# Performance work log

Measured on AMD Instinct MI355X. Metric: run time of the kernel, lower is better.

Reference implementation:

```python
import jax, jax.numpy as jnp
import numpy as np

B = 4096        # number of motif graphs in the batch
H = 256         # hidden_channels
P = 128         # num_prototypes
V = 2000        # motif vocab size (embedding table has V+1 rows)
N_ATOMS = 32768 # focal context atoms
N_RES = 262144  # residues
KNN = 4         # construct_num_neighbors (and cos_sim topk)
DIST_TH = 6.0


def setup_inputs() -> dict:
    key = jax.random.key(0)
    ks = jax.random.split(key, 14)
    return {
        "h_ctx_focal": jax.random.normal(ks[0], (N_ATOMS, H), jnp.float32),
        "pos_ctx_focal": jax.random.normal(ks[1], (N_ATOMS, 3), jnp.float32) * 5.0,
        "h_residue": jax.random.normal(ks[2], (N_RES, H), jnp.float32),
        "residue_pos": jax.random.normal(ks[3], (N_RES, 3, 3), jnp.float32) * 3.0,
        "embedding_weight": jax.random.normal(ks[4], (V + 1, H), jnp.float32) * 0.02,
        "prototypes": jax.random.normal(ks[5], (P, H), jnp.float32),
        "prototype_count": jax.random.uniform(ks[6], (P, V), jnp.float32) * 10.0,
        "motif_w": jax.random.normal(ks[7], (3 * H, H), jnp.float32) * 0.02,
        "motif_b": jnp.zeros((H,), jnp.float32),
        "gnn_w1": jax.random.normal(ks[8], (H, H), jnp.float32) * 0.05,
        "gnn_w2": jax.random.normal(ks[9], (H, H), jnp.float32) * 0.05,
        "current_wid": jax.random.randint(ks[10], (B,), 0, V),
        "current_atoms_batch": jnp.sort(jax.random.randint(ks[11], (N_ATOMS,), 0, B)),
        "amino_acid_batch": jnp.sort(jax.random.randint(ks[12], (N_RES,), 0, B)),
    }


def _l2norm(x, axis=-1):
    # F.normalize: x / max(||x||, eps)
    n = jnp.linalg.norm(x, axis=axis, keepdims=True)
    return x / jnp.maximum(n, 1e-12)


def reference(h_ctx_focal, pos_ctx_focal, h_residue, residue_pos,
              embedding_weight, prototypes, prototype_count,
              motif_w, motif_b, gnn_w1, gnn_w2,
              current_wid, current_atoms_batch, amino_acid_batch):
    # --- scatter-based motif aggregation (forward_motif) ---
    node_hiddens = jax.ops.segment_sum(h_ctx_focal, current_atoms_batch, num_segments=B)
    motif_hiddens = embedding_weight[current_wid]                       # [B,H]
    pos_sum = jax.ops.segment_sum(pos_ctx_focal, current_atoms_batch, num_segments=B)
    cnt = jax.ops.segment_sum(jnp.ones((N_ATOMS,), pos_ctx_focal.dtype),
                              current_atoms_batch, num_segments=B)
    center_pos = pos_sum / jnp.maximum(cnt, 1.0)[:, None]               # scatter_mean [B,3]

    # distance-thresholded residue gather-reduce (CA atom = index 1)
    ca = residue_pos[:, 1, :]                                           # [N_RES,3]
    dist = jnp.linalg.norm(ca - center_pos[amino_acid_batch], axis=1)
    rmask = (dist < DIST_TH).astype(h_residue.dtype)                    # [N_RES]
    residue_emb = jax.ops.segment_sum(h_residue * rmask[:, None],
                                      amino_acid_batch, num_segments=B)  # [B,H]

    # --- MGraph.output: prototype kNN graph + prototype->motif tf-idf edges ---
    cos = _l2norm(residue_emb) @ _l2norm(prototypes).T                  # [B,P]
    _, knn_idx = jax.lax.top_k(cos, KNN)                                # [B,KNN]
    dim = B + P + V
    adj = jnp.zeros((dim, dim), residue_emb.dtype)
    ind1 = knn_idx.T.reshape(-1) + B
    ind0 = jnp.tile(jnp.arange(B), KNN)
    adj = adj.at[ind0, ind1].set(1.0)
    sum_proto = jnp.sum(prototype_count, axis=1, keepdims=True)         # [P,1]
    sum_motif = jnp.sum((prototype_count > 0).astype(jnp.float32), axis=0)  # [V]
    block = prototype_count / (sum_proto + 1.0) * (
        jnp.log((1.0 + P) / (1.0 + sum_motif)) + 1.0)                   # [P,V]
    adj = adj.at[B:B + P, B + P:].set(block)
    A = adj + adj.T  # edge duplication with swapped indices == symmetrize

    # --- WeightGNN (2-layer weighted message passing over the motif graph) ---
    node_feat = jnp.concatenate([residue_emb, prototypes, embedding_weight[:V]], axis=0)
    h1 = jax.nn.relu((A @ node_feat) @ gnn_w1)
    residue_out = ((A @ h1) @ gnn_w2)[:B]                               # [B,H]

    # --- prediction head ---
    pred_vecs = jnp.concatenate([0.8 * node_hiddens,
                                 0.7 * motif_hiddens,
                                 1.5 * residue_out], axis=-1)           # [B,3H]
    pred_scores = (pred_vecs @ motif_w + motif_b) @ embedding_weight.T  # [B,V+1]
    return pred_scores
```

## Files before the change

### kernel.cpp

```cpp
#include <hip/hip_runtime.h>
#include <hip/hip_bf16.h>
#include <math.h>

#define NB 4096
#define HD 256
#define NP 128
#define NV 2000
#define NATOMS 32768
#define NRES 262144
#define VCHUNK 125

typedef __attribute__((ext_vector_type(8))) short bf16x8;
typedef __attribute__((ext_vector_type(4))) float f32x4;
typedef __attribute__((ext_vector_type(8))) unsigned short u16x8;

__device__ __forceinline__ unsigned short f2bf(float f) {
  unsigned int u = __builtin_bit_cast(unsigned int, f);
  u += 0x7FFFu + ((u >> 16) & 1u);
  return (unsigned short)(u >> 16);
}
__device__ __forceinline__ float bf2f(unsigned short h) {
  unsigned int u = ((unsigned int)h) << 16;
  return __builtin_bit_cast(float, u);
}

#define I_SP   128
#define I_WL   (I_SP + 8)
#define I_PR   (I_WL + 128)
#define I_HZ   (I_PR + 128)
#define I_ES   (I_HZ + 512)
#define I_MS   (I_ES + 192)
#define I_AS   (I_MS + 128)
#define I_RS   (I_AS + 1024)

__global__ __launch_bounds__(256) void k_init0(
    const int* __restrict__ ab, const int* __restrict__ rb,
    const float* __restrict__ pcnt, const float* __restrict__ proto,
    const float* __restrict__ emb, const float* __restrict__ mw,
    float* __restrict__ inv_sp, float* __restrict__ wl, float* __restrict__ pnT,
    float* __restrict__ hin,
    unsigned short* __restrict__ embH, unsigned short* __restrict__ embL,
    unsigned short* __restrict__ mwTH, unsigned short* __restrict__ mwTL,
    int* __restrict__ astart, int* __restrict__ rstart) {
  int blk = blockIdx.x, t = threadIdx.x;
  __shared__ float red[256];
  if (blk < I_SP) {
    int p = blk;
    float s = 0.f;
    for (int v = t; v < NV; v += 256) s += pcnt[(size_t)p * NV + v];
    red[t] = s; __syncthreads();
    for (int off = 128; off; off >>= 1) { if (t < off) red[t] += red[t + off]; __syncthreads(); }
    if (!t) inv_sp[p] = 1.0f / (red[0] + 1.0f);
  } else if (blk < I_WL) {
    int v = (blk - I_SP) * 256 + t;
    if (v < NV) {
      float sm = 0.f;
      for (int p = 0; p < NP; ++p) sm += (pcnt[(size_t)p * NV + v] > 0.f) ? 1.f : 0.f;
      wl[v] = logf((1.0f + NP) / (1.0f + sm)) + 1.0f;
    }
  } else if (blk < I_PR) {
    int p = blk - I_WL;
    float x = proto[p * HD + t];
    red[t] = x * x; __syncthreads();
    for (int off = 128; off; off >>= 1) { if (t < off) red[t] += red[t + off]; __syncthreads(); }
    float inv = 1.0f / fmaxf(sqrtf(red[0]), 1e-12f);
    pnT[t * NP + p] = x * inv;
  } else if (blk < I_HZ) {
    hin[(blk - I_PR) * 256 + t] = 0.f;
  } else if (blk < I_ES) {
    int e0 = ((blk - I_HZ) * 256 + t) * 4;
#pragma unroll
    for (int j = 0; j < 4; ++j) {
      int e = e0 + j;
      if (e < 2001 * HD) {
        float x = emb[e];
        unsigned short h = f2bf(x);
        embH[e] = h; embL[e] = f2bf(x - bf2f(h));
      } else {
        embH[e] = 0; embL[e] = 0;
      }
    }
  } else if (blk < I_MS) {
    int e0 = ((blk - I_ES) * 256 + t) * 4;
#pragma unroll
    for (int j = 0; j < 4; ++j) {
      int e = e0 + j;
      int n = e / 768, k = e - n * 768;
      float x = mw[(size_t)k * HD + n];
      unsigned short h = f2bf(x);
      mwTH[e] = h; mwTL[e] = f2bf(x - bf2f(h));
    }
  } else if (blk < I_AS) {
    int i = (blk - I_MS) * 256 + t;
    int cur = ab[i];
    int prev = (i == 0) ? -1 : ab[i - 1];
    for (int b = prev + 1; b <= cur; ++b) astart[b] = i;
    if (i == NATOMS - 1)
      for (int b = cur + 1; b <= NB; ++b) astart[b] = NATOMS;
  } else {
    int i = (blk - I_AS) * 256 + t;
    int cur = rb[i];
    int prev = (i == 0) ? -1 : rb[i - 1];
    for (int b = prev + 1; b <= cur; ++b) rstart[b] = i;
    if (i == NRES - 1)
      for (int b = cur + 1; b <= NB; ++b) rstart[b] = NRES;
  }
}

__global__ __launch_bounds__(256) void k_mega(
    const float* __restrict__ hctx, const float* __restrict__ pos,
    const float* __restrict__ hres, const float* __restrict__ rpos,
    const int* __restrict__ astart, const int* __restrict__ rstart,
    const float* __restrict__ pcnt, const float* __restrict__ wl,
    const float* __restrict__ inv_sp, const float* __restrict__ emb,
    const float* __restrict__ pnT,
    float* __restrict__ nh, int* __restrict__ knn, float* __restrict__ hin) {
  int blk = blockIdx.x, t = threadIdx.x;
  __shared__ int lst[256];
  __shared__ int cnt;
  __shared__ float cw[VCHUNK];
  __shared__ float sre[HD];
  __shared__ float part[256];
  __shared__ float c[NP];
  __shared__ float rv[256];
  __shared__ int ri[256];
  __shared__ int kk[4];
  __shared__ float scen[3];
  if (blk < NB) {
    int b = blk;
    int s = astart[b], e = astart[b + 1];
    {
      float a0 = 0.f, a1 = 0.f, a2 = 0.f, a3 = 0.f;
      int a = s;
      for (; a + 3 < e; a += 4) {
        a0 += hctx[(size_t)(a + 0) * HD + t];
        a1 += hctx[(size_t)(a + 1) * HD + t];
        a2 += hctx[(size_t)(a + 2) * HD + t];
        a3 += hctx[(size_t)(a + 3) * HD + t];
      }
      for (; a < e; ++a) a0 += hctx[(size_t)a * HD + t];
      nh[(size_t)b * HD + t] = (a0 + a1) + (a2 + a3);
      if (t < 3) {
        float ps = 0.f;
        for (int aa = s; aa < e; ++aa) ps += pos[aa * 3 + t];
        scen[t] = ps / fmaxf((float)(e - s), 1.0f);
      }
    }
    __syncthreads();
    float c0 = scen[0], c1 = scen[1], c2 = scen[2];
    int rs = rstart[b], re_ = rstart[b + 1];
    float a0 = 0.f, a1 = 0.f, a2 = 0.f, a3 = 0.f, a4 = 0.f, a5 = 0.f, a6 = 0.f, a7 = 0.f;
    for (int cc = rs; cc < re_; cc += 256) {
      if (!t) cnt = 0;
      __syncthreads();
      int r = cc + t;
      if (r < re_) {
        float dx = rpos[(size_t)r * 9 + 3] - c0;
        float dy = rpos[(size_t)r * 9 + 4] - c1;
        float dz = rpos[(size_t)r * 9 + 5] - c2;
        if (dx * dx + dy * dy + dz * dz < 36.0f) {
          int j = atomicAdd(&cnt, 1);
          lst[j] = r;
        }
      }
      __syncthreads();
      int n = cnt;
      int j = 0;
      for (; j + 7 < n; j += 8) {
        a0 += hres[(size_t)lst[j + 0] * HD + t];
        a1 += hres[(size_t)lst[j + 1] * HD + t];
        a2 += hres[(size_t)lst[j + 2] * HD + t];
        a3 += hres[(size_t)lst[j + 3] * HD + t];
        a4 += hres[(size_t)lst[j + 4] * HD + t];
        a5 += hres[(size_t)lst[j + 5] * HD + t];
        a6 += hres[(size_t)lst[j + 6] * HD + t];
        a7 += hres[(size_t)lst[j + 7] * HD + t];
      }
      for (; j < n; ++j) a0 += hres[(size_t)lst[j] * HD + t];
      __syncthreads();
    }
    float acc = ((a0 + a1) + (a2 + a3)) + ((a4 + a5) + (a6 + a7));
    sre[t] = acc;
    part[t] = acc * acc;
    __syncthreads();
    for (int off = 128; off; off >>= 1) { if (t < off) part[t] += part[t + off]; __syncthreads(); }
    float invn = 1.0f / fmaxf(sqrtf(part[0]), 1e-12f);
    __syncthreads();
    int p = t & 127, half = t >> 7;
    float d = 0.f;
    int h0 = half * 128;
#pragma unroll 8
    for (int h = h0; h < h0 + 128; ++h) d += sre[h] * pnT[h * NP + p];
    part[t] = d;
    __syncthreads();
    if (t < NP) c[t] = (part[t] + part[t + 128]) * invn;
    __syncthreads();
    for (int k = 0; k < 4; ++k) {
      rv[t] = (t < NP) ? c[t] : -INFINITY;
      ri[t] = t;
      __syncthreads();
      for (int off = 128; off; off >>= 1) {
        if (t < off) {
          float ov = rv[t + off]; int oi = ri[t + off];
          if (ov > rv[t] || (ov == rv[t] && oi < ri[t])) { rv[t] = ov; ri[t] = oi; }
        }
        __syncthreads();
      }
      if (!t) { knn[b * 4 + k] = ri[0]; kk[k] = ri[0]; }
      if (t == ri[0]) c[t] = -INFINITY;
      __syncthreads();
    }
#pragma unroll
    for (int k = 0; k < 4; ++k) atomicAdd(&hin[kk[k] * HD + t], sre[t]);
  } else {
    int pc = blk - NB;
    int p = pc >> 4, ch = pc & 15;
    int v0 = ch * VCHUNK;
    float isp = inv_sp[p];
    for (int v = t; v < VCHUNK; v += 256) cw[v] = pcnt[(size_t)p * NV + v0 + v] * wl[v0 + v] * isp;
    __syncthreads();
    float acc = 0.f;
#pragma unroll 8
    for (int v = 0; v < VCHUNK; ++v) acc += cw[v] * emb[(size_t)(v0 + v) * HD + t];
    atomicAdd(&hin[p * HD + t], acc);
  }
}

__global__ __launch_bounds__(256) void k_h1hw(const float* __restrict__ hin,
                                              const float* __restrict__ w1,
                                              const float* __restrict__ w2,
                                              float* __restrict__ hw) {
  int p = blockIdx.x, t = threadIdx.x;
  __shared__ float s[HD], s2[HD];
  s[t] = hin[p * HD + t];
  __syncthreads();
  float a = 0.f;
#pragma unroll 8
  for (int h = 0; h < HD; ++h) a += s[h] * w1[h * HD + t];
  s2[t] = fmaxf(a, 0.f);
  __syncthreads();
  float o = 0.f;
#pragma unroll 8
  for (int h = 0; h < HD; ++h) o += s2[h] * w2[h * HD + t];
  hw[p * HD + t] = o;
}

__global__ __launch_bounds__(512) void k_gemm1(
    const float* __restrict__ nh, const float* __restrict__ emb,
    const int* __restrict__ wid, const int* __restrict__ knn, const float* __restrict__ hw,
    const unsigned short* __restrict__ mwTH, const unsigned short* __restrict__ mwTL,
    const float* __restrict__ mb,
    unsigned short* __restrict__ tbH, unsigned short* __restrict__ tbL) {
  __shared__ __align__(16) unsigned short Ah[64][40], Al[64][40], Bh[64][40], Bl[64][40];
  __shared__ int swid[64];
  __shared__ int4 sknn[64];
  int tid = threadIdx.x, lane = tid & 63, w = tid >> 6;
  int wm = (w & 1) * 32, wn = (w >> 1) * 16;
  int bm = blockIdx.x * 64, bn = blockIdx.y * 64;
  if (tid < 64) { swid[tid] = wid[bm + tid]; sknn[tid] = ((const int4*)knn)[bm + tid]; }
  f32x4 acc[2] = {};
  for (int k0 = 0; k0 < 768; k0 += 32) {
    __syncthreads();
    for (int i = tid; i < 2048; i += 512) {
      int m = i >> 5, k = i & 31;
      float x;
      if (k0 < 256) {
        x = 0.8f * nh[(size_t)(bm + m) * HD + k0 + k];
      } else if (k0 < 512) {
        x = 0.7f * emb[(size_t)swid[m] * HD + (k0 - 256) + k];
      } else {
        int4 kn = sknn[m];
        int kk2 = (k0 - 512) + k;
        x = 1.5f * (hw[kn.x * HD + kk2] + hw[kn.y * HD + kk2] +
                    hw[kn.z * HD + kk2] + hw[kn.w * HD + kk2]);
      }
      unsigned short h = f2bf(x);
      Ah[m][k] = h; Al[m][k] = f2bf(x - bf2f(h));
    }
    if (tid < 256) {
      int e = tid * 8, n = e >> 5, k = e & 31;
      size_t idx = (size_t)(bn + n) * 768 + k0 + k;
      *(u16x8*)&Bh[n][k] = *(const u16x8*)&mwTH[idx];
      *(u16x8*)&Bl[n][k] = *(const u16x8*)&mwTL[idx];
    }
    __syncthreads();
    int r = lane & 15, kb = (lane >> 4) * 8;
    bf16x8 bh = *(const bf16x8*)&Bh[wn + r][kb];
    bf16x8 bl = *(const bf16x8*)&Bl[wn + r][kb];
#pragma unroll
    for (int i = 0; i < 2; ++i) {
      bf16x8 ah = *(const bf16x8*)&Ah[wm + i * 16 + r][kb];
      bf16x8 al = *(const bf16x8*)&Al[wm + i * 16 + r][kb];
      acc[i] = __builtin_amdgcn_mfma_f32_16x16x32_bf16(ah, bh, acc[i], 0, 0, 0);
      acc[i] = __builtin_amdgcn_mfma_f32_16x16x32_bf16(ah, bl, acc[i], 0, 0, 0);
      acc[i] = __builtin_amdgcn_mfma_f32_16x16x32_bf16(al, bh, acc[i], 0, 0, 0);
    }
  }
  int col0 = lane & 15, row0 = (lane >> 4) * 4;
  int col = bn + wn + col0;
  float bv = mb[col];
#pragma unroll
  for (int i = 0; i < 2; ++i)
#pragma unroll
    for (int rr = 0; rr < 4; ++rr) {
      int row = bm + wm + i * 16 + row0 + rr;
      float x = acc[i][rr] + bv;
      unsigned short h = f2bf(x);
      tbH[(size_t)row * HD + col] = h;
      tbL[(size_t)row * HD + col] = f2bf(x - bf2f(h));
    }
}

__global__ __launch_bounds__(256) void k_gemm2(
    const unsigned short* __restrict__ tbH, const unsigned short* __restrict__ tbL,
    const unsigned short* __restrict__ embH, const unsigned short* __restrict__ embL,
    float* __restrict__ out) {
  __shared__ __align__(16) unsigned short AH[128][40], AL[128][40], BH[128][40], BL[128][40];
  int tid = threadIdx.x, lane = tid & 63, w = tid >> 6;
  int wm = (w & 1) * 64, wn = (w >> 1) * 64;
  int orig = blockIdx.x;
  int swz = (orig & 7) * 64 + (orig >> 3);
  int bm = (swz & 31) * 128, bn = (swz >> 5) * 128;
  f32x4 acc[4][4] = {};
  for (int k0 = 0; k0 < HD; k0 += 32) {
    __syncthreads();
#pragma unroll
    for (int cch = 0; cch < 2; ++cch) {
      int e = (tid + cch * 256) * 8;
      int m = e >> 5, k = e & 31;
      *(u16x8*)&AH[m][k] = *(const u16x8*)&tbH[(size_t)(bm + m) * HD + k0 + k];
      *(u16x8*)&AL[m][k] = *(const u16x8*)&tbL[(size_t)(bm + m) * HD + k0 + k];
      *(u16x8*)&BH[m][k] = *(const u16x8*)&embH[(size_t)(bn + m) * HD + k0 + k];
      *(u16x8*)&BL[m][k] = *(const u16x8*)&embL[(size_t)(bn + m) * HD + k0 + k];
    }
    __syncthreads();
    int r = lane & 15, kb = (lane >> 4) * 8;
    bf16x8 ah[4], al[4], bh[4], bl[4];
#pragma unroll
    for (int i = 0; i < 4; ++i) {
      ah[i] = *(const bf16x8*)&AH[wm + i * 16 + r][kb];
      al[i] = *(const bf16x8*)&AL[wm + i * 16 + r][kb];
      bh[i] = *(const bf16x8*)&BH[wn + i * 16 + r][kb];
      bl[i] = *(const bf16x8*)&BL[wn + i * 16 + r][kb];
    }
#pragma unroll
    for (int i = 0; i < 4; ++i)
#pragma unroll
      for (int j = 0; j < 4; ++j) {
        acc[i][j] = __builtin_amdgcn_mfma_f32_16x16x32_bf16(ah[i], bh[j], acc[i][j], 0, 0, 0);
        acc[i][j] = __builtin_amdgcn_mfma_f32_16x16x32_bf16(ah[i], bl[j], acc[i][j], 0, 0, 0);
        acc[i][j] = __builtin_amdgcn_mfma_f32_16x16x32_bf16(al[i], bh[j], acc[i][j], 0, 0, 0);
      }
  }
  int col0 = lane & 15, row0 = (lane >> 4) * 4;
#pragma unroll
  for (int i = 0; i < 4; ++i)
#pragma unroll
    for (int j = 0; j < 4; ++j) {
      int col = bn + wn + j * 16 + col0;
      if (col <= 2000) {
#pragma unroll
        for (int rr = 0; rr < 4; ++rr) {
          int row = bm + wm + i * 16 + row0 + rr;
          out[(size_t)row * 2001 + col] = acc[i][j][rr];
        }
      }
    }
}

extern "C" void kernel_launch(void* const* d_in, const int* in_sizes, int n_in,
                              void* d_out, int out_size, void* d_ws, size_t ws_size,
                              hipStream_t stream) {
  const float* hctx  = (const float*)d_in[0];
  const float* pos   = (const float*)d_in[1];
  const float* hres  = (const float*)d_in[2];
  const float* rpos  = (const float*)d_in[3];
  const float* emb   = (const float*)d_in[4];
  const float* proto = (const float*)d_in[5];
  const float* pcnt  = (const float*)d_in[6];
  const float* mw    = (const float*)d_in[7];
  const float* mb    = (const float*)d_in[8];
  const float* w1    = (const float*)d_in[9];
  const float* w2    = (const float*)d_in[10];
  const int* wid     = (const int*)d_in[11];
  const int* ab      = (const int*)d_in[12];
  const int* rb      = (const int*)d_in[13];
  float* out = (float*)d_out;

  float* ws     = (float*)d_ws;
  float* nh     = ws;
  float* inv_sp = nh + (size_t)NB * HD;
  float* wl     = inv_sp + 128;
  float* pnT    = wl + 2048;
  float* hin    = pnT + NP * HD;
  float* hw     = hin + NP * HD;
  int*   knn    = (int*)(hw + NP * HD);
  int*   astart = knn + NB * 4;
  int*   rstart = astart + 4104;
  unsigned short* tbH  = (unsigned short*)(rstart + 4104);
  unsigned short* tbL  = tbH + (size_t)NB * HD;
  unsigned short* embH = tbL + (size_t)NB * HD;
  unsigned short* embL = embH + (size_t)2048 * HD;
  unsigned short* mwTH = embL + (size_t)2048 * HD;
  unsigned short* mwTL = mwTH + (size_t)768 * HD;

  k_init0<<<I_RS, 256, 0, stream>>>(ab, rb, pcnt, proto, emb, mw,
                                    inv_sp, wl, pnT, hin,
                                    embH, embL, mwTH, mwTL, astart, rstart);
  k_mega<<<NB + NP * 16, 256, 0, stream>>>(hctx, pos, hres, rpos, astart, rstart,
                                           pcnt, wl, inv_sp, emb, pnT, nh, knn, hin);
  k_h1hw<<<NP, 256, 0, stream>>>(hin, w1, w2, hw);
  k_gemm1<<<dim3(NB / 64, 4), 512, 0, stream>>>(nh, emb, wid, knn, hw,
                                                mwTH, mwTL, mb, tbH, tbL);
  k_gemm2<<<512, 256, 0, stream>>>(tbH, tbL, embH, embL, out);
}
```

Measured before the change: 534.9 us.

## Use wave shuffles in top-k, split gemm1 prologue, double-buffer both GEMMs

New measurement: 513.9 us. 3.9% less time.

```diff
diff --git a/kernel.cpp b/kernel.cpp
--- a/kernel.cpp
+++ b/kernel.cpp
@@ -122,12 +122,12 @@
   __shared__ float sre[HD];
   __shared__ float part[256];
   __shared__ float c[NP];
-  __shared__ float rv[256];
-  __shared__ int ri[256];
+  __shared__ float wsum[4];
   __shared__ int kk[4];
   __shared__ float scen[3];
   if (blk < NB) {
     int b = blk;
+    int lane = t & 63, w = t >> 6;
     int s = astart[b], e = astart[b + 1];
     {
       float a0 = 0.f, a1 = 0.f, a2 = 0.f, a3 = 0.f;
@@ -181,11 +181,12 @@
     }
     float acc = ((a0 + a1) + (a2 + a3)) + ((a4 + a5) + (a6 + a7));
     sre[t] = acc;
-    part[t] = acc * acc;
-    __syncthreads();
-    for (int off = 128; off; off >>= 1) { if (t < off) part[t] += part[t + off]; __syncthreads(); }
-    float invn = 1.0f / fmaxf(sqrtf(part[0]), 1e-12f);
-    __syncthreads();
+    float ss = acc * acc;
+#pragma unroll
+    for (int off = 32; off; off >>= 1) ss += __shfl_xor(ss, off);
+    if (!lane) wsum[w] = ss;
+    __syncthreads();
+    float invn = 1.0f / fmaxf(sqrtf((wsum[0] + wsum[1]) + (wsum[2] + wsum[3])), 1e-12f);
     int p = t & 127, half = t >> 7;
     float d = 0.f;
     int h0 = half * 128;
@@ -195,21 +196,24 @@
     __syncthreads();
     if (t < NP) c[t] = (part[t] + part[t + 128]) * invn;
     __syncthreads();
-    for (int k = 0; k < 4; ++k) {
-      rv[t] = (t < NP) ? c[t] : -INFINITY;
-      ri[t] = t;
-      __syncthreads();
-      for (int off = 128; off; off >>= 1) {
-        if (t < off) {
-          float ov = rv[t + off]; int oi = ri[t + off];
-          if (ov > rv[t] || (ov == rv[t] && oi < ri[t])) { rv[t] = ov; ri[t] = oi; }
+    if (t < 64) {
+      float v0 = c[t], v1 = c[t + 64];
+#pragma unroll
+      for (int k = 0; k < 4; ++k) {
+        float bv = v0; int bi = t;
+        if (v1 > bv) { bv = v1; bi = t + 64; }
+#pragma unroll
+        for (int off = 32; off; off >>= 1) {
+          float ov = __shfl_xor(bv, off);
+          int oi = __shfl_xor(bi, off);
+          if (ov > bv || (ov == bv && oi < bi)) { bv = ov; bi = oi; }
         }
-        __syncthreads();
-      }
-      if (!t) { knn[b * 4 + k] = ri[0]; kk[k] = ri[0]; }
-      if (t == ri[0]) c[t] = -INFINITY;
-      __syncthreads();
-    }
+        if (!t) { knn[b * 4 + k] = bi; kk[k] = bi; }
+        if (bi == t) v0 = -INFINITY;
+        if (bi == t + 64) v1 = -INFINITY;
+      }
+    }
+    __syncthreads();
 #pragma unroll
     for (int k = 0; k < 4; ++k) atomicAdd(&hin[kk[k] * HD + t], sre[t]);
   } else {
@@ -245,69 +249,83 @@
   hw[p * HD + t] = o;
 }
 
-__global__ __launch_bounds__(512) void k_gemm1(
+__global__ __launch_bounds__(256) void k_prepU(
     const float* __restrict__ nh, const float* __restrict__ emb,
     const int* __restrict__ wid, const int* __restrict__ knn, const float* __restrict__ hw,
+    unsigned short* __restrict__ uH, unsigned short* __restrict__ uL) {
+  int b = blockIdx.x, t = threadIdx.x;
+  size_t base = (size_t)b * 768;
+  float x0 = 0.8f * nh[(size_t)b * HD + t];
+  float x1 = 0.7f * emb[(size_t)wid[b] * HD + t];
+  int4 kn = ((const int4*)knn)[b];
+  float x2 = 1.5f * (hw[kn.x * HD + t] + hw[kn.y * HD + t] +
+                     hw[kn.z * HD + t] + hw[kn.w * HD + t]);
+  unsigned short h;
+  h = f2bf(x0); uH[base + t] = h;       uL[base + t] = f2bf(x0 - bf2f(h));
+  h = f2bf(x1); uH[base + 256 + t] = h; uL[base + 256 + t] = f2bf(x1 - bf2f(h));
+  h = f2bf(x2); uH[base + 512 + t] = h; uL[base + 512 + t] = f2bf(x2 - bf2f(h));
+}
+
+__global__ __launch_bounds__(256) void k_gemm1(
+    const unsigned short* __restrict__ uH, const unsigned short* __restrict__ uL,
     const unsigned short* __restrict__ mwTH, const unsigned short* __restrict__ mwTL,
     const float* __restrict__ mb,
     unsigned short* __restrict__ tbH, unsigned short* __restrict__ tbL) {
-  __shared__ __align__(16) unsigned short Ah[64][40], Al[64][40], Bh[64][40], Bl[64][40];
-  __shared__ int swid[64];
-  __shared__ int4 sknn[64];
+  __shared__ __align__(16) unsigned short AH[2][64][40], AL[2][64][40],
+                                          BH[2][64][40], BL[2][64][40];
   int tid = threadIdx.x, lane = tid & 63, w = tid >> 6;
-  int wm = (w & 1) * 32, wn = (w >> 1) * 16;
+  int wm = (w & 1) * 32, wn = (w >> 1) * 32;
   int bm = blockIdx.x * 64, bn = blockIdx.y * 64;
-  if (tid < 64) { swid[tid] = wid[bm + tid]; sknn[tid] = ((const int4*)knn)[bm + tid]; }
-  f32x4 acc[2] = {};
-  for (int k0 = 0; k0 < 768; k0 += 32) {
-    __syncthreads();
-    for (int i = tid; i < 2048; i += 512) {
-      int m = i >> 5, k = i & 31;
-      float x;
-      if (k0 < 256) {
-        x = 0.8f * nh[(size_t)(bm + m) * HD + k0 + k];
-      } else if (k0 < 512) {
-        x = 0.7f * emb[(size_t)swid[m] * HD + (k0 - 256) + k];
-      } else {
-        int4 kn = sknn[m];
-        int kk2 = (k0 - 512) + k;
-        x = 1.5f * (hw[kn.x * HD + kk2] + hw[kn.y * HD + kk2] +
-                    hw[kn.z * HD + kk2] + hw[kn.w * HD + kk2]);
-      }
-      unsigned short h = f2bf(x);
-      Ah[m][k] = h; Al[m][k] = f2bf(x - bf2f(h));
-    }
-    if (tid < 256) {
-      int e = tid * 8, n = e >> 5, k = e & 31;
-      size_t idx = (size_t)(bn + n) * 768 + k0 + k;
-      *(u16x8*)&Bh[n][k] = *(const u16x8*)&mwTH[idx];
-      *(u16x8*)&Bl[n][k] = *(const u16x8*)&mwTL[idx];
-    }
-    __syncthreads();
+  f32x4 acc[2][2] = {};
+#define G1_STAGE(bf, kt)                                                        \
+  {                                                                             \
+    int e = tid * 8, m = e >> 5, k = e & 31;                                    \
+    size_t ia = (size_t)(bm + m) * 768 + (kt) * 32 + k;                         \
+    size_t ib = (size_t)(bn + m) * 768 + (kt) * 32 + k;                         \
+    *(u16x8*)&AH[bf][m][k] = *(const u16x8*)&uH[ia];                            \
+    *(u16x8*)&AL[bf][m][k] = *(const u16x8*)&uL[ia];                            \
+    *(u16x8*)&BH[bf][m][k] = *(const u16x8*)&mwTH[ib];                          \
+    *(u16x8*)&BL[bf][m][k] = *(const u16x8*)&mwTL[ib];                          \
+  }
+  G1_STAGE(0, 0);
+  __syncthreads();
+  for (int kt = 0; kt < 24; ++kt) {
+    int cur = kt & 1;
+    if (kt + 1 < 24) G1_STAGE(cur ^ 1, kt + 1);
     int r = lane & 15, kb = (lane >> 4) * 8;
-    bf16x8 bh = *(const bf16x8*)&Bh[wn + r][kb];
-    bf16x8 bl = *(const bf16x8*)&Bl[wn + r][kb];
+    bf16x8 ah[2], al[2], bh[2], bl[2];
 #pragma unroll
     for (int i = 0; i < 2; ++i) {
-      bf16x8 ah = *(const bf16x8*)&Ah[wm + i * 16 + r][kb];
-      bf16x8 al = *(const bf16x8*)&Al[wm + i * 16 + r][kb];
-      acc[i] = __builtin_amdgcn_mfma_f32_16x16x32_bf16(ah, bh, acc[i], 0, 0, 0);
-      acc[i] = __builtin_amdgcn_mfma_f32_16x16x32_bf16(ah, bl, acc[i], 0, 0, 0);
-      acc[i] = __builtin_amdgcn_mfma_f32_16x16x32_bf16(al, bh, acc[i], 0, 0, 0);
-    }
+      ah[i] = *(const bf16x8*)&AH[cur][wm + i * 16 + r][kb];
+      al[i] = *(const bf16x8*)&AL[cur][wm + i * 16 + r][kb];
+      bh[i] = *(const bf16x8*)&BH[cur][wn + i * 16 + r][kb];
+      bl[i] = *(const bf16x8*)&BL[cur][wn + i * 16 + r][kb];
+    }
+#pragma unroll
+    for (int i = 0; i < 2; ++i)
+#pragma unroll
+      for (int j = 0; j < 2; ++j) {
+        acc[i][j] = __builtin_amdgcn_mfma_f32_16x16x32_bf16(ah[i], bh[j], acc[i][j], 0, 0, 0);
+        acc[i][j] = __builtin_amdgcn_mfma_f32_16x16x32_bf16(ah[i], bl[j], acc[i][j], 0, 0, 0);
+        acc[i][j] = __builtin_amdgcn_mfma_f32_16x16x32_bf16(al[i], bh[j], acc[i][j], 0, 0, 0);
+      }
+    __syncthreads();
   }
   int col0 = lane & 15, row0 = (lane >> 4) * 4;
-  int col = bn + wn + col0;
-  float bv = mb[col];
 #pragma unroll
   for (int i = 0; i < 2; ++i)
 #pragma unroll
-    for (int rr = 0; rr < 4; ++rr) {
-      int row = bm + wm + i * 16 + row0 + rr;
-      float x = acc[i][rr] + bv;
-      unsigned short h = f2bf(x);
-      tbH[(size_t)row * HD + col] = h;
-      tbL[(size_t)row * HD + col] = f2bf(x - bf2f(h));
+    for (int j = 0; j < 2; ++j) {
+      int col = bn + wn + j * 16 + col0;
+      float bv = mb[col];
+#pragma unroll
+      for (int rr = 0; rr < 4; ++rr) {
+        int row = bm + wm + i * 16 + row0 + rr;
+        float x = acc[i][j][rr] + bv;
+        unsigned short h = f2bf(x);
+        tbH[(size_t)row * HD + col] = h;
+        tbL[(size_t)row * HD + col] = f2bf(x - bf2f(h));
+      }
     }
 }
 
@@ -315,33 +333,41 @@
     const unsigned short* __restrict__ tbH, const unsigned short* __restrict__ tbL,
     const unsigned short* __restrict__ embH, const unsigned short* __restrict__ embL,
     float* __restrict__ out) {
-  __shared__ __align__(16) unsigned short AH[128][40], AL[128][40], BH[128][40], BL[128][40];
+  __shared__ __align__(16) unsigned short AH[2][128][40], AL[2][128][40],
+                                          BH[2][128][40], BL[2][128][40];
   int tid = threadIdx.x, lane = tid & 63, w = tid >> 6;
   int wm = (w & 1) * 64, wn = (w >> 1) * 64;
   int orig = blockIdx.x;
   int swz = (orig & 7) * 64 + (orig >> 3);
   int bm = (swz & 31) * 128, bn = (swz >> 5) * 128;
   f32x4 acc[4][4] = {};
-  for (int k0 = 0; k0 < HD; k0 += 32) {
-    __syncthreads();
-#pragma unroll
-    for (int cch = 0; cch < 2; ++cch) {
-      int e = (tid + cch * 256) * 8;
-      int m = e >> 5, k = e & 31;
-      *(u16x8*)&AH[m][k] = *(const u16x8*)&tbH[(size_t)(bm + m) * HD + k0 + k];
-      *(u16x8*)&AL[m][k] = *(const u16x8*)&tbL[(size_t)(bm + m) * HD + k0 + k];
-      *(u16x8*)&BH[m][k] = *(const u16x8*)&embH[(size_t)(bn + m) * HD + k0 + k];
-      *(u16x8*)&BL[m][k] = *(const u16x8*)&embL[(size_t)(bn + m) * HD + k0 + k];
-    }
-    __syncthreads();
+#define G2_STAGE(bf, kt)                                                        \
+  {                                                                             \
+    _Pragma("unroll")                                                           \
+    for (int cch = 0; cch < 2; ++cch) {                                         \
+      int e = (tid + cch * 256) * 8;                                            \
+      int m = e >> 5, k = e & 31;                                               \
+      size_t ia = (size_t)(bm + m) * HD + (kt) * 32 + k;                        \
+      size_t ib = (size_t)(bn + m) * HD + (kt) * 32 + k;                        \
+      *(u16x8*)&AH[bf][m][k] = *(const u16x8*)&tbH[ia];                         \
+      *(u16x8*)&AL[bf][m][k] = *(const u16x8*)&tbL[ia];                         \
+      *(u16x8*)&BH[bf][m][k] = *(const u16x8*)&embH[ib];                        \
+      *(u16x8*)&BL[bf][m][k] = *(const u16x8*)&embL[ib];                        \
+    }                                                                           \
+  }
+  G2_STAGE(0, 0);
+  __syncthreads();
+  for (int kt = 0; kt < 8; ++kt) {
+    int cur = kt & 1;
+    if (kt + 1 < 8) G2_STAGE(cur ^ 1, kt + 1);
     int r = lane & 15, kb = (lane >> 4) * 8;
     bf16x8 ah[4], al[4], bh[4], bl[4];
 #pragma unroll
     for (int i = 0; i < 4; ++i) {
-      ah[i] = *(const bf16x8*)&AH[wm + i * 16 + r][kb];
-      al[i] = *(const bf16x8*)&AL[wm + i * 16 + r][kb];
-      bh[i] = *(const bf16x8*)&BH[wn + i * 16 + r][kb];
-      bl[i] = *(const bf16x8*)&BL[wn + i * 16 + r][kb];
+      ah[i] = *(const bf16x8*)&AH[cur][wm + i * 16 + r][kb];
+      al[i] = *(const bf16x8*)&AL[cur][wm + i * 16 + r][kb];
+      bh[i] = *(const bf16x8*)&BH[cur][wn + i * 16 + r][kb];
+      bl[i] = *(const bf16x8*)&BL[cur][wn + i * 16 + r][kb];
     }
 #pragma unroll
     for (int i = 0; i < 4; ++i)
@@ -351,6 +377,7 @@
         acc[i][j] = __builtin_amdgcn_mfma_f32_16x16x32_bf16(ah[i], bl[j], acc[i][j], 0, 0, 0);
         acc[i][j] = __builtin_amdgcn_mfma_f32_16x16x32_bf16(al[i], bh[j], acc[i][j], 0, 0, 0);
       }
+    __syncthreads();
   }
   int col0 = lane & 15, row0 = (lane >> 4) * 4;
 #pragma unroll
@@ -403,6 +430,8 @@
   unsigned short* embL = embH + (size_t)2048 * HD;
   unsigned short* mwTH = embL + (size_t)2048 * HD;
   unsigned short* mwTL = mwTH + (size_t)768 * HD;
+  unsigned short* uH   = mwTL + (size_t)768 * HD;
+  unsigned short* uL   = uH + (size_t)NB * 768;
 
   k_init0<<<I_RS, 256, 0, stream>>>(ab, rb, pcnt, proto, emb, mw,
                                     inv_sp, wl, pnT, hin,
@@ -410,7 +439,7 @@
   k_mega<<<NB + NP * 16, 256, 0, stream>>>(hctx, pos, hres, rpos, astart, rstart,
                                            pcnt, wl, inv_sp, emb, pnT, nh, knn, hin);
   k_h1hw<<<NP, 256, 0, stream>>>(hin, w1, w2, hw);
-  k_gemm1<<<dim3(NB / 64, 4), 512, 0, stream>>>(nh, emb, wid, knn, hw,
-                                                mwTH, mwTL, mb, tbH, tbL);
+  k_prepU<<<NB, 256, 0, stream>>>(nh, emb, wid, knn, hw, uH, uL);
+  k_gemm1<<<dim3(NB / 64, 4), 256, 0, stream>>>(uH, uL, mwTH, mwTL, mb, tbH, tbL);
   k_gemm2<<<512, 256, 0, stream>>>(tbH, tbL, embH, embL, out);
 }
```
